# Kernel optimization log

Measured on AMD Instinct MI355X. Metric: run time of the kernel, lower is better.

Reference implementation:

```python
import jax, jax.numpy as jnp
import numpy as np

B, S, E, H = 2, 2048, 512, 8
D = E // H  # head size = 64
LN_EPS = 1e-5


def setup_inputs() -> dict:
    key = jax.random.key(0)
    ks = jax.random.split(key, 8)
    s_in = 1.0 / np.sqrt(E)
    return {
        "x": jax.random.normal(ks[0], (B, S, E), jnp.float32),
        # per-head projection weights, stored [H, E, D] so q = x @ Wq[h]
        "Wq": jax.random.normal(ks[1], (H, E, D), jnp.float32) * s_in,
        "Wk": jax.random.normal(ks[2], (H, E, D), jnp.float32) * s_in,
        "Wv": jax.random.normal(ks[3], (H, E, D), jnp.float32) * s_in,
        "Wp": jax.random.normal(ks[4], (E, E), jnp.float32) * s_in,
        "bp": jnp.zeros((E,), jnp.float32),
        "gamma": jnp.ones((E,), jnp.float32),
        "beta": jnp.zeros((E,), jnp.float32),
        # causal mask buffer: masked_fill where mask == 0
        "mask": jnp.tril(jnp.ones((S, S), jnp.int32)),
    }


def reference(x, Wq, Wk, Wv, Wp, bp, gamma, beta, mask):
    # batched per-head projections (equivalent to the H small Linears)
    q = jnp.einsum("bse,hed->bhsd", x, Wq)
    k = jnp.einsum("bse,hed->bhsd", x, Wk)
    v = jnp.einsum("bse,hed->bhsd", x, Wv)
    # NOTE: original has NO 1/sqrt(d) scaling
    att_log = jnp.einsum("bhsd,bhtd->bhst", q, k)
    att_log = jnp.where(mask == 0, -jnp.inf, att_log)
    att = jax.nn.softmax(att_log, axis=-1)
    o = jnp.einsum("bhst,bhtd->bhsd", att, v)  # [B,H,S,D]
    # torch.cat((val, values)) prepends each head -> final order head H-1 .. 0
    o = o[:, ::-1]
    vals = o.transpose(0, 2, 1, 3).reshape(B, S, E)
    out = vals @ Wp.T + bp + x
    mu = jnp.mean(out, axis=-1, keepdims=True)
    var = jnp.var(out, axis=-1, keepdims=True)
    return (out - mu) * jax.lax.rsqrt(var + LN_EPS) * gamma + beta
```

## Files before the change

kernel.cpp:

```cpp
#include <hip/hip_runtime.h>

constexpr int Bn = 2;
constexpr int Sn = 2048;
constexpr int En = 512;
constexpr int Hn = 8;
constexpr int Dn = 64;
constexpr int Mn = Bn * Sn;

typedef short bf8 __attribute__((ext_vector_type(8)));
typedef float f32x4 __attribute__((ext_vector_type(4)));

constexpr size_t XY = (size_t)Mn * En;
constexpr size_t WT = (size_t)3 * En * En;
constexpr size_t WP = (size_t)En * En;
constexpr size_t PL = (size_t)Bn * Hn * Sn * Dn;

__device__ __forceinline__ unsigned short f2bf(float f) {
    unsigned int u = __float_as_uint(f);
    unsigned int r = 0x7FFFu + ((u >> 16) & 1u);
    return (unsigned short)((u + r) >> 16);
}
__device__ __forceinline__ float bf2f(unsigned short u) {
    return __uint_as_float(((unsigned int)u) << 16);
}
__device__ __forceinline__ void split2(float f, unsigned short& hi, unsigned short& lo) {
    hi = f2bf(f);
    lo = f2bf(f - bf2f(hi));
}

__global__ __launch_bounds__(256)
void prep(const float* __restrict__ x, const float* __restrict__ Wp,
          const float* __restrict__ Wq, const float* __restrict__ Wk,
          const float* __restrict__ Wv,
          unsigned short* __restrict__ xh, unsigned short* __restrict__ xl,
          unsigned short* __restrict__ Wph, unsigned short* __restrict__ Wpl,
          unsigned short* __restrict__ Wth, unsigned short* __restrict__ Wtl)
{
    __shared__ float t[64][65];
    const int bid = blockIdx.x;
    const int tid = threadIdx.x;

    if (bid < 1152) {
        const float* src = (bid < 1024) ? x : Wp;
        unsigned short* hp = (bid < 1024) ? xh : Wph;
        unsigned short* lp = (bid < 1024) ? xl : Wpl;
        const int blk = (bid < 1024) ? bid : (bid - 1024);
        const size_t base = ((size_t)blk * 256 + tid) * 8;
        float a[8];
        *(float4*)&a[0] = *(const float4*)(src + base);
        *(float4*)&a[4] = *(const float4*)(src + base + 4);
        unsigned short h[8], l[8];
        #pragma unroll
        for (int j = 0; j < 8; ++j) split2(a[j], h[j], l[j]);
        *(bf8*)(hp + base) = *(bf8*)&h[0];
        *(bf8*)(lp + base) = *(bf8*)&l[0];
        return;
    }

    const int idx = bid - 1152;
    const int ph = idx >> 3;
    const int proj = ph >> 3, h = ph & 7;
    const int e0 = (idx & 7) * 64;
    const float* W = (proj == 0) ? Wq : (proj == 1) ? Wk : Wv;
    const float* src = W + (size_t)h * En * Dn + (size_t)e0 * Dn;

    const int er = tid >> 2, cg = (tid & 3) * 16;
    #pragma unroll
    for (int c = 0; c < 4; ++c) {
        float4 v = *(const float4*)(src + (size_t)er * Dn + cg + 4 * c);
        t[er][cg + 4 * c + 0] = v.x;
        t[er][cg + 4 * c + 1] = v.y;
        t[er][cg + 4 * c + 2] = v.z;
        t[er][cg + 4 * c + 3] = v.w;
    }
    __syncthreads();

    const int d = tid >> 2, jg = (tid & 3) * 16;
    unsigned short h16[16], l16[16];
    #pragma unroll
    for (int j = 0; j < 16; ++j) split2(t[jg + j][d], h16[j], l16[j]);
    const size_t n = (size_t)proj * 512 + h * 64 + d;
    unsigned short* dh = Wth + n * En + e0 + jg;
    unsigned short* dl = Wtl + n * En + e0 + jg;
    *(bf8*)dh       = *(bf8*)&h16[0];
    *(bf8*)(dh + 8) = *(bf8*)&h16[8];
    *(bf8*)dl       = *(bf8*)&l16[0];
    *(bf8*)(dl + 8) = *(bf8*)&l16[8];
}

__global__ __launch_bounds__(256)
void qkv_gemm(const unsigned short* __restrict__ xh,
              const unsigned short* __restrict__ xl,
              const unsigned short* __restrict__ Wth,
              const unsigned short* __restrict__ Wtl,
              unsigned short* __restrict__ qh_g,
              unsigned short* __restrict__ ql_g,
              unsigned short* __restrict__ kh_g,
              unsigned short* __restrict__ kl_g,
              unsigned short* __restrict__ vT_g)
{
    __shared__ __align__(16) unsigned char smraw[30720];
    unsigned short (*Ah)[40] = (unsigned short(*)[40])(smraw);
    unsigned short (*Al)[40] = (unsigned short(*)[40])(smraw + 10240);
    unsigned short (*Bh)[40] = (unsigned short(*)[40])(smraw + 20480);
    unsigned short (*Bl)[40] = (unsigned short(*)[40])(smraw + 25600);
    float (*Cf)[68] = (float(*)[68])(smraw);

    const int tid = threadIdx.x;
    const int m0 = blockIdx.x * 128;
    const int ny = blockIdx.y;
    const int proj = ny >> 3, h = ny & 7;

    const int wave = tid >> 6, lane = tid & 63;
    const int wm = (wave >> 1) * 64, wn = (wave & 1) * 32;
    const int lm = lane & 15, quad = lane >> 4;

    const int am = tid >> 1;
    const int aks = (tid & 1) * 16;
    const unsigned short* arh = xh + (size_t)(m0 + am) * En + aks;
    const unsigned short* arl = xl + (size_t)(m0 + am) * En + aks;

    const int bn = tid >> 2;
    const int bks = (tid & 3) * 8;
    const unsigned short* brh = Wth + (size_t)(ny * 64 + bn) * En + bks;
    const unsigned short* brl = Wtl + (size_t)(ny * 64 + bn) * En + bks;

    f32x4 acc[4][2];
    #pragma unroll
    for (int i = 0; i < 4; ++i)
        #pragma unroll
        for (int j = 0; j < 2; ++j) acc[i][j] = (f32x4){0.f, 0.f, 0.f, 0.f};

    for (int k0 = 0; k0 < En; k0 += 32) {
        *(bf8*)&Ah[am][aks]     = *(const bf8*)(arh + k0);
        *(bf8*)&Ah[am][aks + 8] = *(const bf8*)(arh + k0 + 8);
        *(bf8*)&Al[am][aks]     = *(const bf8*)(arl + k0);
        *(bf8*)&Al[am][aks + 8] = *(const bf8*)(arl + k0 + 8);
        *(bf8*)&Bh[bn][bks]     = *(const bf8*)(brh + k0);
        *(bf8*)&Bl[bn][bks]     = *(const bf8*)(brl + k0);
        __syncthreads();

        bf8 a_h[4], a_l[4], b_h[2], b_l[2];
        #pragma unroll
        for (int mi = 0; mi < 4; ++mi) {
            a_h[mi] = *(const bf8*)&Ah[wm + mi * 16 + lm][quad * 8];
            a_l[mi] = *(const bf8*)&Al[wm + mi * 16 + lm][quad * 8];
        }
        #pragma unroll
        for (int ni = 0; ni < 2; ++ni) {
            b_h[ni] = *(const bf8*)&Bh[wn + ni * 16 + lm][quad * 8];
            b_l[ni] = *(const bf8*)&Bl[wn + ni * 16 + lm][quad * 8];
        }
        #pragma unroll
        for (int mi = 0; mi < 4; ++mi)
            #pragma unroll
            for (int ni = 0; ni < 2; ++ni) {
                acc[mi][ni] = __builtin_amdgcn_mfma_f32_16x16x32_bf16(a_h[mi], b_h[ni], acc[mi][ni], 0, 0, 0);
                acc[mi][ni] = __builtin_amdgcn_mfma_f32_16x16x32_bf16(a_h[mi], b_l[ni], acc[mi][ni], 0, 0, 0);
                acc[mi][ni] = __builtin_amdgcn_mfma_f32_16x16x32_bf16(a_l[mi], b_h[ni], acc[mi][ni], 0, 0, 0);
            }
        __syncthreads();
    }

    if (proj < 2) {
        unsigned short* hp = (proj == 0) ? qh_g : kh_g;
        unsigned short* lp = (proj == 0) ? ql_g : kl_g;
        #pragma unroll
        for (int p = 0; p < 2; ++p) {
            if ((wave >> 1) == p) {
                #pragma unroll
                for (int mi = 0; mi < 4; ++mi)
                    #pragma unroll
                    for (int ni = 0; ni < 2; ++ni)
                        #pragma unroll
                        for (int r = 0; r < 4; ++r)
                            Cf[mi * 16 + quad * 4 + r][wn + ni * 16 + lm] = acc[mi][ni][r];
            }
            __syncthreads();
            {
                const int lr = tid & 63;
                const int cg = (tid >> 6) * 16;
                const int m = m0 + p * 64 + lr;
                const int b = m >> 11, s = m & 2047;
                unsigned short hi[16], lo[16];
                #pragma unroll
                for (int j4 = 0; j4 < 4; ++j4) {
                    float4 v = *(const float4*)&Cf[lr][cg + 4 * j4];
                    split2(v.x, hi[4 * j4 + 0], lo[4 * j4 + 0]);
                    split2(v.y, hi[4 * j4 + 1], lo[4 * j4 + 1]);
                    split2(v.z, hi[4 * j4 + 2], lo[4 * j4 + 2]);
                    split2(v.w, hi[4 * j4 + 3], lo[4 * j4 + 3]);
                }
                const size_t base = (((size_t)(b * Hn + h) * Sn + s) * Dn) + cg;
                *(bf8*)(hp + base)     = *(bf8*)&hi[0];
                *(bf8*)(hp + base + 8) = *(bf8*)&hi[8];
                *(bf8*)(lp + base)     = *(bf8*)&lo[0];
                *(bf8*)(lp + base + 8) = *(bf8*)&lo[8];
            }
            __syncthreads();
        }
    } else {
        #pragma unroll
        for (int mi = 0; mi < 4; ++mi) {
            const int s0 = m0 + wm + mi * 16 + quad * 4;
            const int b = s0 >> 11, s = s0 & 2047;
            #pragma unroll
            for (int ni = 0; ni < 2; ++ni) {
                const int d = wn + ni * 16 + lm;
                ushort4 pk;
                pk.x = f2bf(acc[mi][ni][0]);
                pk.y = f2bf(acc[mi][ni][1]);
                pk.z = f2bf(acc[mi][ni][2]);
                pk.w = f2bf(acc[mi][ni][3]);
                *(ushort4*)(vT_g + ((size_t)(b * Hn + h) * Dn + d) * Sn + s) = pk;
            }
        }
    }
}

__global__ __launch_bounds__(256)
void attn(const unsigned short* __restrict__ qh_g,
          const unsigned short* __restrict__ ql_g,
          const unsigned short* __restrict__ kh_g,
          const unsigned short* __restrict__ kl_g,
          const unsigned short* __restrict__ vT_g,
          unsigned short* __restrict__ Op,
          float* __restrict__ ml)
{
    extern __shared__ unsigned short sm[];
    unsigned short (*khs)[72] = (unsigned short(*)[72])(sm);
    unsigned short (*kls)[72] = (unsigned short(*)[72])(sm + 4608);
    unsigned short (*vTs)[72] = (unsigned short(*)[72])(sm + 9216);
    unsigned short (*pts)[72] = (unsigned short(*)[72])(sm + 13824);
    float* alf = (float*)(sm + 18432);

    const int bidx = blockIdx.x;
    const int xcd = bidx & 7;
    const int g = bidx >> 3;
    const int bh = xcd * 2 + (g & 1);
    const int rest = g >> 1;
    const int hf = rest >> 5;
    const int a_ = rest & 31;
    const int qt = hf ? (31 - a_) : a_;
    const int n0 = (qt + 2) >> 1;
    const int its = hf ? n0 : 0;
    const int ite = hf ? (qt + 1) : n0;
    const int pslot = hf * 512 + bh * 32 + qt;

    const int tid = threadIdx.x;
    const int wave = tid >> 6, lane = tid & 63;
    const int quad = lane >> 4, lq = lane & 15;

    const unsigned short* khb = kh_g + (size_t)bh * Sn * Dn;
    const unsigned short* klb = kl_g + (size_t)bh * Sn * Dn;
    const unsigned short* vTb = vT_g + (size_t)bh * Dn * Sn;

    bf8 qfh[2], qfl[2];
    {
        const size_t qoff = ((size_t)bh * Sn + (size_t)qt * 64 + wave * 16 + lq) * Dn;
        #pragma unroll
        for (int c = 0; c < 2; ++c) {
            qfh[c] = *(const bf8*)(qh_g + qoff + c * 32 + quad * 8);
            qfl[c] = *(const bf8*)(ql_g + qoff + c * 32 + quad * 8);
        }
    }

    f32x4 accO[4];
    #pragma unroll
    for (int nj = 0; nj < 4; ++nj) accO[nj] = (f32x4){0.f, 0.f, 0.f, 0.f};
    float m = -1e30f, l = 0.f;

    const int srow = tid & 63;
    const int sdg  = tid >> 6;

    bf8 pk0, pk1, pl0, pl1, pv0, pv1;
    if (its < ite) {
        const int t0 = its * 64;
        const unsigned short* kr = khb + (size_t)(t0 + srow) * Dn + sdg * 16;
        const unsigned short* lr = klb + (size_t)(t0 + srow) * Dn + sdg * 16;
        const unsigned short* vr = vTb + (size_t)srow * Sn + t0 + sdg * 16;
        pk0 = *(const bf8*)(kr);  pk1 = *(const bf8*)(kr + 8);
        pl0 = *(const bf8*)(lr);  pl1 = *(const bf8*)(lr + 8);
        pv0 = *(const bf8*)(vr);  pv1 = *(const bf8*)(vr + 8);
    }

    for (int it = its; it < ite; ++it) {
        __syncthreads();
        *(bf8*)&khs[srow][sdg * 16]     = pk0;
        *(bf8*)&khs[srow][sdg * 16 + 8] = pk1;
        *(bf8*)&kls[srow][sdg * 16]     = pl0;
        *(bf8*)&kls[srow][sdg * 16 + 8] = pl1;
        *(bf8*)&vTs[srow][sdg * 16]     = pv0;
        *(bf8*)&vTs[srow][sdg * 16 + 8] = pv1;
        __syncthreads();

        if (it + 1 < ite) {
            const int t1 = (it + 1) * 64;
            const unsigned short* kr = khb + (size_t)(t1 + srow) * Dn + sdg * 16;
            const unsigned short* lr = klb + (size_t)(t1 + srow) * Dn + sdg * 16;
            const unsigned short* vr = vTb + (size_t)srow * Sn + t1 + sdg * 16;
            pk0 = *(const bf8*)(kr);  pk1 = *(const bf8*)(kr + 8);
            pl0 = *(const bf8*)(lr);  pl1 = *(const bf8*)(lr + 8);
            pv0 = *(const bf8*)(vr);  pv1 = *(const bf8*)(vr + 8);
        }

        f32x4 accS[4];
        #pragma unroll
        for (int mi = 0; mi < 4; ++mi) accS[mi] = (f32x4){0.f, 0.f, 0.f, 0.f};
        #pragma unroll
        for (int mi = 0; mi < 4; ++mi) {
            #pragma unroll
            for (int c = 0; c < 2; ++c) {
                bf8 ah = *(const bf8*)&khs[mi * 16 + lq][c * 32 + quad * 8];
                bf8 al = *(const bf8*)&kls[mi * 16 + lq][c * 32 + quad * 8];
                accS[mi] = __builtin_amdgcn_mfma_f32_16x16x32_bf16(ah, qfh[c], accS[mi], 0, 0, 0);
                accS[mi] = __builtin_amdgcn_mfma_f32_16x16x32_bf16(ah, qfl[c], accS[mi], 0, 0, 0);
                accS[mi] = __builtin_amdgcn_mfma_f32_16x16x32_bf16(al, qfh[c], accS[mi], 0, 0, 0);
            }
        }

        if (it == qt) {
            const int qrel = wave * 16 + lq;
            #pragma unroll
            for (int mi = 0; mi < 4; ++mi)
                #pragma unroll
                for (int r = 0; r < 4; ++r)
                    if (mi * 16 + quad * 4 + r > qrel) accS[mi][r] = -INFINITY;
        }

        float mt = -INFINITY;
        #pragma unroll
        for (int mi = 0; mi < 4; ++mi)
            #pragma unroll
            for (int r = 0; r < 4; ++r) mt = fmaxf(mt, accS[mi][r]);
        mt = fmaxf(mt, __shfl_xor(mt, 16));
        mt = fmaxf(mt, __shfl_xor(mt, 32));
        const float mnew = fmaxf(m, mt);
        const float alpha = __expf(m - mnew);
        float ls = 0.f;
        #pragma unroll
        for (int mi = 0; mi < 4; ++mi)
            #pragma unroll
            for (int r = 0; r < 4; ++r) {
                const float p = __expf(accS[mi][r] - mnew);
                accS[mi][r] = p;
                ls += p;
            }
        ls += __shfl_xor(ls, 16);
        ls += __shfl_xor(ls, 32);
        l = l * alpha + ls;
        m = mnew;

        #pragma unroll
        for (int mi = 0; mi < 4; ++mi) {
            ushort4 pk;
            pk.x = f2bf(accS[mi][0]);
            pk.y = f2bf(accS[mi][1]);
            pk.z = f2bf(accS[mi][2]);
            pk.w = f2bf(accS[mi][3]);
            *(ushort4*)&pts[wave * 16 + lq][mi * 16 + quad * 4] = pk;
        }
        if (quad == 0) alf[wave * 16 + lq] = alpha;

        {
            float4 al4 = *(const float4*)&alf[wave * 16 + quad * 4];
            #pragma unroll
            for (int nj = 0; nj < 4; ++nj) {
                accO[nj][0] *= al4.x;
                accO[nj][1] *= al4.y;
                accO[nj][2] *= al4.z;
                accO[nj][3] *= al4.w;
            }
            #pragma unroll
            for (int c = 0; c < 2; ++c) {
                bf8 pf = *(const bf8*)&pts[wave * 16 + lq][c * 32 + quad * 8];
                #pragma unroll
                for (int nj = 0; nj < 4; ++nj) {
                    bf8 vf = *(const bf8*)&vTs[nj * 16 + lq][c * 32 + quad * 8];
                    accO[nj] = __builtin_amdgcn_mfma_f32_16x16x32_bf16(pf, vf, accO[nj], 0, 0, 0);
                }
            }
        }
    }

    if (quad == 0) {
        const size_t mi_ = ((size_t)pslot * 64 + wave * 16 + lq) * 2;
        ml[mi_]     = m;
        ml[mi_ + 1] = l;
    }
    #pragma unroll
    for (int r = 0; r < 4; ++r) {
        const int q = wave * 16 + quad * 4 + r;
        unsigned short* dst = Op + ((size_t)pslot * 64 + q) * 64;
        #pragma unroll
        for (int nj = 0; nj < 4; ++nj)
            dst[nj * 16 + lq] = f2bf(accO[nj][r]);
    }
}

__global__ __launch_bounds__(256)
void out_gemm(const unsigned short* __restrict__ Op,
              const float* __restrict__ ml,
              const unsigned short* __restrict__ Wph,
              const unsigned short* __restrict__ Wpl,
              const float* __restrict__ bp,
              const float* __restrict__ x,
              float* __restrict__ outp,
              float* __restrict__ outp2)
{
    __shared__ unsigned short Ah[64][40], Al[64][40];
    __shared__ unsigned short Bh[128][40], Bl[128][40];

    const int tid = threadIdx.x;
    const int m0 = blockIdx.x * 64;
    const int n0 = blockIdx.y * 128;
    const int kz = blockIdx.z;
    const int kbeg = kz * 256, kend = kbeg + 256;

    const int wave = tid >> 6, lane = tid & 63;
    const int wm = (wave >> 1) * 32, wn = (wave & 1) * 64;
    const int lm = lane & 15, quad = lane >> 4;

    const int am = tid >> 2;
    const int aks = (tid & 3) * 8;
    const int m_row = m0 + am;
    const int b_row = m_row >> 11, s_row = m_row & 2047;
    const int qt = s_row >> 6, qq = s_row & 63;

    float c0[8], c1[8];
    #pragma unroll
    for (int h = 0; h < 8; ++h) {
        const size_t base0 = (((size_t)(b_row * 8 + h) * 32 + qt) * 64 + qq) * 2;
        const size_t base1 = base0 + (size_t)512 * 64 * 2;
        const float m0_ = ml[base0], l0_ = ml[base0 + 1];
        const float m1_ = ml[base1], l1_ = ml[base1 + 1];
        const float mn = fmaxf(m0_, m1_);
        const float a0 = __expf(m0_ - mn), a1 = __expf(m1_ - mn);
        const float inv = 1.f / (a0 * l0_ + a1 * l1_);
        c0[h] = a0 * inv;
        c1[h] = a1 * inv;
    }

    const int bn = tid >> 1;
    const int bks = (tid & 1) * 16;
    const unsigned short* brh = Wph + (size_t)(n0 + bn) * En + bks;
    const unsigned short* brl = Wpl + (size_t)(n0 + bn) * En + bks;

    f32x4 acc[2][4];
    #pragma unroll
    for (int i = 0; i < 2; ++i)
        #pragma unroll
        for (int j = 0; j < 4; ++j) acc[i][j] = (f32x4){0.f, 0.f, 0.f, 0.f};

    for (int k0 = kbeg; k0 < kend; k0 += 32) {
        {
            const int e0 = k0 + aks;
            const int h = 7 - (e0 >> 6);
            const int d = e0 & 63;
            const size_t p0 = (((size_t)((b_row * 8 + h) * 32 + qt)) * 64 + qq) * 64 + d;
            const size_t p1 = p0 + (size_t)512 * 64 * 64;
            bf8 o0 = *(const bf8*)(Op + p0);
            bf8 o1 = *(const bf8*)(Op + p1);
            const float w0 = c0[h], w1 = c1[h];
            unsigned short hi[8], lo[8];
            #pragma unroll
            for (int j = 0; j < 8; ++j) {
                const float v = w0 * bf2f((unsigned short)o0[j]) +
                                w1 * bf2f((unsigned short)o1[j]);
                split2(v, hi[j], lo[j]);
            }
            *(bf8*)&Ah[am][aks] = *(bf8*)&hi[0];
            *(bf8*)&Al[am][aks] = *(bf8*)&lo[0];
        }
        *(bf8*)&Bh[bn][bks]     = *(const bf8*)(brh + k0);
        *(bf8*)&Bh[bn][bks + 8] = *(const bf8*)(brh + k0 + 8);
        *(bf8*)&Bl[bn][bks]     = *(const bf8*)(brl + k0);
        *(bf8*)&Bl[bn][bks + 8] = *(const bf8*)(brl + k0 + 8);
        __syncthreads();

        bf8 a_h[2], a_l[2], b_h[4], b_l[4];
        #pragma unroll
        for (int mi = 0; mi < 2; ++mi) {
            a_h[mi] = *(const bf8*)&Ah[wm + mi * 16 + lm][quad * 8];
            a_l[mi] = *(const bf8*)&Al[wm + mi * 16 + lm][quad * 8];
        }
        #pragma unroll
        for (int ni = 0; ni < 4; ++ni) {
            b_h[ni] = *(const bf8*)&Bh[wn + ni * 16 + lm][quad * 8];
            b_l[ni] = *(const bf8*)&Bl[wn + ni * 16 + lm][quad * 8];
        }
        #pragma unroll
        for (int mi = 0; mi < 2; ++mi)
            #pragma unroll
            for (int ni = 0; ni < 4; ++ni) {
                acc[mi][ni] = __builtin_amdgcn_mfma_f32_16x16x32_bf16(a_h[mi], b_h[ni], acc[mi][ni], 0, 0, 0);
                acc[mi][ni] = __builtin_amdgcn_mfma_f32_16x16x32_bf16(a_h[mi], b_l[ni], acc[mi][ni], 0, 0, 0);
                acc[mi][ni] = __builtin_amdgcn_mfma_f32_16x16x32_bf16(a_l[mi], b_h[ni], acc[mi][ni], 0, 0, 0);
            }
        __syncthreads();
    }

    float* dst = kz ? outp2 : outp;
    #pragma unroll
    for (int mi = 0; mi < 2; ++mi) {
        #pragma unroll
        for (int r = 0; r < 4; ++r) {
            const int m = m0 + wm + mi * 16 + quad * 4 + r;
            #pragma unroll
            for (int ni = 0; ni < 4; ++ni) {
                const int n = n0 + wn + ni * 16 + lm;
                const size_t idx = (size_t)m * En + n;
                const float extra = kz ? 0.f : (bp[n] + x[idx]);
                dst[idx] = acc[mi][ni][r] + extra;
            }
        }
    }
}

__global__ __launch_bounds__(256)
void ln_kernel(const float* __restrict__ outp,
               const float* __restrict__ outp2,
               const float* __restrict__ gamma,
               const float* __restrict__ beta,
               float* __restrict__ y)
{
    const int row = blockIdx.x * 4 + (threadIdx.x >> 6);
    const int lane = threadIdx.x & 63;
    const size_t off = (size_t)row * En + lane * 8;

    float a[8], b2[8];
    *(float4*)&a[0] = *(const float4*)(outp + off);
    *(float4*)&a[4] = *(const float4*)(outp + off + 4);
    *(float4*)&b2[0] = *(const float4*)(outp2 + off);
    *(float4*)&b2[4] = *(const float4*)(outp2 + off + 4);
    #pragma unroll
    for (int j = 0; j < 8; ++j) a[j] += b2[j];

    float sum = 0.f, sq = 0.f;
    #pragma unroll
    for (int j = 0; j < 8; ++j) { sum += a[j]; sq += a[j] * a[j]; }
    #pragma unroll
    for (int off_ = 1; off_ < 64; off_ <<= 1) {
        sum += __shfl_xor(sum, off_);
        sq  += __shfl_xor(sq, off_);
    }
    const float mu = sum * (1.f / 512.f);
    const float var = sq * (1.f / 512.f) - mu * mu;
    const float rs = rsqrtf(var + 1e-5f);

    const float* g = gamma + lane * 8;
    const float* be = beta + lane * 8;
    float o[8];
    #pragma unroll
    for (int j = 0; j < 8; ++j)
        o[j] = (a[j] - mu) * rs * g[j] + be[j];
    float* yr = y + off;
    *(float4*)(yr)     = *(float4*)&o[0];
    *(float4*)(yr + 4) = *(float4*)&o[4];
}

extern "C" void kernel_launch(void* const* d_in, const int* in_sizes, int n_in,
                              void* d_out, int out_size, void* d_ws, size_t ws_size,
                              hipStream_t stream)
{
    const float* x     = (const float*)d_in[0];
    const float* Wq    = (const float*)d_in[1];
    const float* Wk    = (const float*)d_in[2];
    const float* Wv    = (const float*)d_in[3];
    const float* Wp    = (const float*)d_in[4];
    const float* bp    = (const float*)d_in[5];
    const float* gamma = (const float*)d_in[6];
    const float* beta  = (const float*)d_in[7];

    float* ws   = (float*)d_ws;
    float* ml   = ws;
    float* outp = ws + XY;
    unsigned short* bfb = (unsigned short*)(ws + 2 * XY);
    unsigned short* xh  = bfb;
    unsigned short* xl  = bfb + XY;
    unsigned short* Wth = bfb + 2 * XY;
    unsigned short* Wtl = Wth + WT;
    unsigned short* Wph = Wtl + WT;
    unsigned short* Wpl = Wph + WP;
    unsigned short* qh  = Wpl + WP;
    unsigned short* ql  = qh + PL;
    unsigned short* kh  = ql + PL;
    unsigned short* kl  = kh + PL;
    unsigned short* vT  = kl + PL;
    unsigned short* Op = xh;
    float* outp2 = (float*)qh;

    const int attn_lds = 18432 * 2 + 256;
    hipFuncSetAttribute((const void*)attn,
                        hipFuncAttributeMaxDynamicSharedMemorySize, attn_lds);

    prep<<<dim3(1344), 256, 0, stream>>>(x, Wp, Wq, Wk, Wv,
                                         xh, xl, Wph, Wpl, Wth, Wtl);
    qkv_gemm<<<dim3(Mn / 128, 24), 256, 0, stream>>>(xh, xl, Wth, Wtl,
                                                     qh, ql, kh, kl, vT);
    attn<<<dim3(1024), 256, attn_lds, stream>>>(qh, ql, kh, kl, vT, Op, ml);
    out_gemm<<<dim3(Mn / 64, En / 128, 2), 256, 0, stream>>>(Op, ml, Wph, Wpl,
                                                             bp, x, outp, outp2);
    ln_kernel<<<dim3(Mn / 4), 256, 0, stream>>>(outp, outp2, gamma, beta,
                                                (float*)d_out);
}
```

Baseline: 176.1 us.

## Prefetch GEMM tiles into registers, defer softmax rescale, raise MFMA priority

The QKV projection and output projection GEMMs now load the next K-slice from global memory into registers right after the barrier, so the load overlaps the MFMA work on the current tile. The attention loop adds lazy rescaling: when the new row max stays within 12 of the running max, it keeps the old reference max and skips the alpha rescale of the output accumulator. MFMA sections are wrapped in s_setprio. These changes aim to hide global load latency and cut exp and rescale work, at the cost of extra registers and a data-dependent branch.

```diff
diff --git a/kernel.cpp b/kernel.cpp
--- a/kernel.cpp
+++ b/kernel.cpp
@@ -131,14 +131,30 @@
         #pragma unroll
         for (int j = 0; j < 2; ++j) acc[i][j] = (f32x4){0.f, 0.f, 0.f, 0.f};
 
+    bf8 pah0 = *(const bf8*)(arh);
+    bf8 pah1 = *(const bf8*)(arh + 8);
+    bf8 pal0 = *(const bf8*)(arl);
+    bf8 pal1 = *(const bf8*)(arl + 8);
+    bf8 pbh0 = *(const bf8*)(brh);
+    bf8 pbl0 = *(const bf8*)(brl);
+
     for (int k0 = 0; k0 < En; k0 += 32) {
-        *(bf8*)&Ah[am][aks]     = *(const bf8*)(arh + k0);
-        *(bf8*)&Ah[am][aks + 8] = *(const bf8*)(arh + k0 + 8);
-        *(bf8*)&Al[am][aks]     = *(const bf8*)(arl + k0);
-        *(bf8*)&Al[am][aks + 8] = *(const bf8*)(arl + k0 + 8);
-        *(bf8*)&Bh[bn][bks]     = *(const bf8*)(brh + k0);
-        *(bf8*)&Bl[bn][bks]     = *(const bf8*)(brl + k0);
+        *(bf8*)&Ah[am][aks]     = pah0;
+        *(bf8*)&Ah[am][aks + 8] = pah1;
+        *(bf8*)&Al[am][aks]     = pal0;
+        *(bf8*)&Al[am][aks + 8] = pal1;
+        *(bf8*)&Bh[bn][bks]     = pbh0;
+        *(bf8*)&Bl[bn][bks]     = pbl0;
         __syncthreads();
+
+        if (k0 + 32 < En) {
+            pah0 = *(const bf8*)(arh + k0 + 32);
+            pah1 = *(const bf8*)(arh + k0 + 40);
+            pal0 = *(const bf8*)(arl + k0 + 32);
+            pal1 = *(const bf8*)(arl + k0 + 40);
+            pbh0 = *(const bf8*)(brh + k0 + 32);
+            pbl0 = *(const bf8*)(brl + k0 + 32);
+        }
 
         bf8 a_h[4], a_l[4], b_h[2], b_l[2];
         #pragma unroll
@@ -307,6 +323,7 @@
         f32x4 accS[4];
         #pragma unroll
         for (int mi = 0; mi < 4; ++mi) accS[mi] = (f32x4){0.f, 0.f, 0.f, 0.f};
+        __builtin_amdgcn_s_setprio(1);
         #pragma unroll
         for (int mi = 0; mi < 4; ++mi) {
             #pragma unroll
@@ -318,6 +335,7 @@
                 accS[mi] = __builtin_amdgcn_mfma_f32_16x16x32_bf16(al, qfh[c], accS[mi], 0, 0, 0);
             }
         }
+        __builtin_amdgcn_s_setprio(0);
 
         if (it == qt) {
             const int qrel = wave * 16 + lq;
@@ -328,28 +346,43 @@
                     if (mi * 16 + quad * 4 + r > qrel) accS[mi][r] = -INFINITY;
         }
 
-        float mt = -INFINITY;
-        #pragma unroll
-        for (int mi = 0; mi < 4; ++mi)
-            #pragma unroll
-            for (int r = 0; r < 4; ++r) mt = fmaxf(mt, accS[mi][r]);
+        float mt;
+        {
+            float t0 = fmaxf(fmaxf(accS[0][0], accS[0][1]), fmaxf(accS[0][2], accS[0][3]));
+            float t1 = fmaxf(fmaxf(accS[1][0], accS[1][1]), fmaxf(accS[1][2], accS[1][3]));
+            float t2 = fmaxf(fmaxf(accS[2][0], accS[2][1]), fmaxf(accS[2][2], accS[2][3]));
+            float t3 = fmaxf(fmaxf(accS[3][0], accS[3][1]), fmaxf(accS[3][2], accS[3][3]));
+            mt = fmaxf(fmaxf(t0, t1), fmaxf(t2, t3));
+        }
         mt = fmaxf(mt, __shfl_xor(mt, 16));
         mt = fmaxf(mt, __shfl_xor(mt, 32));
-        const float mnew = fmaxf(m, mt);
-        const float alpha = __expf(m - mnew);
+
+        const bool defer = __all(mt <= m + 12.f);
+        float mref, alpha = 1.f;
+        if (defer) {
+            mref = m;
+        } else {
+            mref = fmaxf(m, mt);
+            alpha = __expf(m - mref);
+        }
+
         float ls = 0.f;
         #pragma unroll
         for (int mi = 0; mi < 4; ++mi)
             #pragma unroll
             for (int r = 0; r < 4; ++r) {
-                const float p = __expf(accS[mi][r] - mnew);
+                const float p = __expf(accS[mi][r] - mref);
                 accS[mi][r] = p;
                 ls += p;
             }
         ls += __shfl_xor(ls, 16);
         ls += __shfl_xor(ls, 32);
-        l = l * alpha + ls;
-        m = mnew;
+        if (defer) {
+            l += ls;
+        } else {
+            l = l * alpha + ls;
+            m = mref;
+        }
 
         #pragma unroll
         for (int mi = 0; mi < 4; ++mi) {
@@ -360,9 +393,9 @@
             pk.w = f2bf(accS[mi][3]);
             *(ushort4*)&pts[wave * 16 + lq][mi * 16 + quad * 4] = pk;
         }
-        if (quad == 0) alf[wave * 16 + lq] = alpha;
-
-        {
+
+        if (!defer) {
+            if (quad == 0) alf[wave * 16 + lq] = alpha;
             float4 al4 = *(const float4*)&alf[wave * 16 + quad * 4];
             #pragma unroll
             for (int nj = 0; nj < 4; ++nj) {
@@ -371,16 +404,19 @@
                 accO[nj][2] *= al4.z;
                 accO[nj][3] *= al4.w;
             }
-            #pragma unroll
-            for (int c = 0; c < 2; ++c) {
-                bf8 pf = *(const bf8*)&pts[wave * 16 + lq][c * 32 + quad * 8];
-                #pragma unroll
-                for (int nj = 0; nj < 4; ++nj) {
-                    bf8 vf = *(const bf8*)&vTs[nj * 16 + lq][c * 32 + quad * 8];
-                    accO[nj] = __builtin_amdgcn_mfma_f32_16x16x32_bf16(pf, vf, accO[nj], 0, 0, 0);
-                }
-            }
-        }
+        }
+
+        __builtin_amdgcn_s_setprio(1);
+        #pragma unroll
+        for (int c = 0; c < 2; ++c) {
+            bf8 pf = *(const bf8*)&pts[wave * 16 + lq][c * 32 + quad * 8];
+            #pragma unroll
+            for (int nj = 0; nj < 4; ++nj) {
+                bf8 vf = *(const bf8*)&vTs[nj * 16 + lq][c * 32 + quad * 8];
+                accO[nj] = __builtin_amdgcn_mfma_f32_16x16x32_bf16(pf, vf, accO[nj], 0, 0, 0);
+            }
+        }
+        __builtin_amdgcn_s_setprio(0);
     }
 
     if (quad == 0) {
@@ -452,31 +488,52 @@
         #pragma unroll
         for (int j = 0; j < 4; ++j) acc[i][j] = (f32x4){0.f, 0.f, 0.f, 0.f};
 
+    bf8 po0, po1, pbh0, pbh1, pbl0, pbl1;
+    {
+        const int e0 = kbeg + aks;
+        const int hh = 7 - (e0 >> 6);
+        const int dd = e0 & 63;
+        const size_t p0 = (((size_t)((b_row * 8 + hh) * 32 + qt)) * 64 + qq) * 64 + dd;
+        po0 = *(const bf8*)(Op + p0);
+        po1 = *(const bf8*)(Op + p0 + (size_t)512 * 64 * 64);
+    }
+    pbh0 = *(const bf8*)(brh + kbeg);
+    pbh1 = *(const bf8*)(brh + kbeg + 8);
+    pbl0 = *(const bf8*)(brl + kbeg);
+    pbl1 = *(const bf8*)(brl + kbeg + 8);
+
     for (int k0 = kbeg; k0 < kend; k0 += 32) {
         {
-            const int e0 = k0 + aks;
-            const int h = 7 - (e0 >> 6);
-            const int d = e0 & 63;
-            const size_t p0 = (((size_t)((b_row * 8 + h) * 32 + qt)) * 64 + qq) * 64 + d;
-            const size_t p1 = p0 + (size_t)512 * 64 * 64;
-            bf8 o0 = *(const bf8*)(Op + p0);
-            bf8 o1 = *(const bf8*)(Op + p1);
-            const float w0 = c0[h], w1 = c1[h];
+            const int h_cur = 7 - ((k0 + aks) >> 6);
+            const float w0 = c0[h_cur], w1 = c1[h_cur];
             unsigned short hi[8], lo[8];
             #pragma unroll
             for (int j = 0; j < 8; ++j) {
-                const float v = w0 * bf2f((unsigned short)o0[j]) +
-                                w1 * bf2f((unsigned short)o1[j]);
+                const float v = w0 * bf2f((unsigned short)po0[j]) +
+                                w1 * bf2f((unsigned short)po1[j]);
                 split2(v, hi[j], lo[j]);
             }
             *(bf8*)&Ah[am][aks] = *(bf8*)&hi[0];
             *(bf8*)&Al[am][aks] = *(bf8*)&lo[0];
         }
-        *(bf8*)&Bh[bn][bks]     = *(const bf8*)(brh + k0);
-        *(bf8*)&Bh[bn][bks + 8] = *(const bf8*)(brh + k0 + 8);
-        *(bf8*)&Bl[bn][bks]     = *(const bf8*)(brl + k0);
-        *(bf8*)&Bl[bn][bks + 8] = *(const bf8*)(brl + k0 + 8);
+        *(bf8*)&Bh[bn][bks]     = pbh0;
+        *(bf8*)&Bh[bn][bks + 8] = pbh1;
+        *(bf8*)&Bl[bn][bks]     = pbl0;
+        *(bf8*)&Bl[bn][bks + 8] = pbl1;
         __syncthreads();
+
+        if (k0 + 32 < kend) {
+            const int e0 = k0 + 32 + aks;
+            const int hh = 7 - (e0 >> 6);
+            const int dd = e0 & 63;
+            const size_t p0 = (((size_t)((b_row * 8 + hh) * 32 + qt)) * 64 + qq) * 64 + dd;
+            po0 = *(const bf8*)(Op + p0);
+            po1 = *(const bf8*)(Op + p0 + (size_t)512 * 64 * 64);
+            pbh0 = *(const bf8*)(brh + k0 + 32);
+            pbh1 = *(const bf8*)(brh + k0 + 40);
+            pbl0 = *(const bf8*)(brl + k0 + 32);
+            pbl1 = *(const bf8*)(brl + k0 + 40);
+        }
 
         bf8 a_h[2], a_l[2], b_h[4], b_l[4];
         #pragma unroll
```

Measured after the change: 175.1 us. No clear change (-0.6%).
